# Kernel optimization log

Hardware: AMD Instinct MI355X
Metric: run time of the kernel (lower is better)

Reference implementation:

```python
import jax, jax.numpy as jnp
import numpy as np

EMBED_DIM = 512
N_HEADS = 8
HEAD_DIM = EMBED_DIM // N_HEADS


def setup_inputs() -> dict:
    key = jax.random.key(0)
    ks = jax.random.split(key, 8)
    B, S, D = 8, 2048, EMBED_DIM
    scale = 1.0 / np.sqrt(D)
    return {
        "key": jax.random.normal(ks[0], (B, S, D), dtype=jnp.float32),
        "query": jax.random.normal(ks[1], (B, S, D), dtype=jnp.float32),
        "value": jax.random.normal(ks[2], (B, S, D), dtype=jnp.float32),
        # nn.Linear stores weight as [out, in]; y = x @ W.T. We store W_T=[in,out].
        "Wq": jax.random.normal(ks[3], (D, D), dtype=jnp.float32) * scale,
        "Wk": jax.random.normal(ks[4], (D, D), dtype=jnp.float32) * scale,
        "Wv": jax.random.normal(ks[5], (D, D), dtype=jnp.float32) * scale,
        "Wo": jax.random.normal(ks[6], (D, D), dtype=jnp.float32) * scale,
        "bo": jax.random.normal(ks[7], (D,), dtype=jnp.float32) * scale,
    }


def reference(key, query, value, Wq, Wk, Wv, Wo, bo):
    B, S, D = key.shape
    Sq = query.shape[1]
    H, Hd = N_HEADS, HEAD_DIM
    # projections (no bias for q/k/v)
    q = (query @ Wq).reshape(B, Sq, H, Hd)
    k = (key @ Wk).reshape(B, S, H, Hd)
    v = (value @ Wv).reshape(B, S, H, Hd)
    # scores: [B, H, Sq, S]
    product = jnp.einsum("bqhd,bkhd->bhqk", q, k) / np.sqrt(Hd)
    scores = jax.nn.softmax(product, axis=-1)
    out = jnp.einsum("bhqk,bkhd->bqhd", scores, v).reshape(B, Sq, D)
    return out @ Wo + bo
```

## Files before the change

kernel.cpp:

```cpp
#include <hip/hip_runtime.h>

typedef _Float16 half8 __attribute__((ext_vector_type(8)));
typedef _Float16 half4 __attribute__((ext_vector_type(4)));
typedef __fp16 fp16x2 __attribute__((ext_vector_type(2)));
typedef float floatx16 __attribute__((ext_vector_type(16)));
typedef unsigned int uint2v __attribute__((ext_vector_type(2)));

#define MFMA_F16 __builtin_amdgcn_mfma_f32_32x32x16_f16

__device__ __forceinline__ float fast_exp2(float x) {
#if __has_builtin(__builtin_amdgcn_exp2f)
    return __builtin_amdgcn_exp2f(x);
#else
    return exp2f(x);
#endif
}

__device__ __forceinline__ half4 pack4(float a, float b, float c, float d) {
    union { fp16x2 p[2]; half4 h; } u;
    u.p[0] = __builtin_amdgcn_cvt_pkrtz(a, b);
    u.p[1] = __builtin_amdgcn_cvt_pkrtz(c, d);
    return u.h;
}

__device__ __forceinline__ unsigned int pk2(float a, float b) {
    union { fp16x2 p; unsigned int u; } v;
    v.p = __builtin_amdgcn_cvt_pkrtz(a, b);
    return v.u;
}

__device__ __forceinline__ half8 ld_frag_lds(const _Float16* p) {
    union { half8 v; half4 h[2]; } u;
    u.h[0] = *(const half4*)(p);
    u.h[1] = *(const half4*)(p + 4);
    return u.v;
}

__device__ __forceinline__ void tile_barrier() {
    asm volatile("s_waitcnt lgkmcnt(0)" ::: "memory");
    __builtin_amdgcn_s_barrier();
    asm volatile("" ::: "memory");
}

__device__ __forceinline__ half8 pv_frag(const unsigned int* w, int i0) {
    uint2v s0 = __builtin_amdgcn_permlane32_swap(w[2 * i0 + 0], w[2 * i0 + 2], false, false);
    uint2v s1 = __builtin_amdgcn_permlane32_swap(w[2 * i0 + 1], w[2 * i0 + 3], false, false);
    union { unsigned int u[4]; half8 h; } pu;
    pu.u[0] = s0[0];
    pu.u[1] = s1[0];
    pu.u[2] = s0[1];
    pu.u[3] = s1[1];
    return pu.h;
}

__global__ __launch_bounds__(256) void wcvt_kernel(const float* __restrict__ Wq,
                                                   const float* __restrict__ Wk,
                                                   const float* __restrict__ Wv,
                                                   const float* __restrict__ Wo,
                                                   _Float16* __restrict__ Wt) {
    __shared__ _Float16 T[64 * 68];
    const int bx   = blockIdx.x;
    const int wsel = bx >> 6;
    const int tile = bx & 63;
    const int to   = (tile >> 3) * 64;
    const int ti   = (tile & 7) * 64;
    const float* src = (wsel == 0) ? Wq : (wsel == 1) ? Wk : (wsel == 2) ? Wv : Wo;
    const int t = threadIdx.x;
    const int rloc = t >> 4, c4 = (t & 15) * 4;
#pragma unroll
    for (int m = 0; m < 4; m++) {
        int i = ti + rloc + 16 * m;
        float4 f = *(const float4*)(src + (size_t)i * 512 + to + c4);
        T[(c4 + 0) * 68 + rloc + 16 * m] = (_Float16)f.x;
        T[(c4 + 1) * 68 + rloc + 16 * m] = (_Float16)f.y;
        T[(c4 + 2) * 68 + rloc + 16 * m] = (_Float16)f.z;
        T[(c4 + 3) * 68 + rloc + 16 * m] = (_Float16)f.w;
    }
    __syncthreads();
    const int o_loc = t >> 2, ich = (t & 3) * 16;
    const _Float16* s = &T[o_loc * 68 + ich];
    _Float16* dst = Wt + (size_t)wsel * 262144 + (size_t)(to + o_loc) * 512 + ti + ich;
    half4 a0 = *(const half4*)(s);
    half4 a1 = *(const half4*)(s + 4);
    half4 a2 = *(const half4*)(s + 8);
    half4 a3 = *(const half4*)(s + 12);
    *(half4*)(dst)      = a0;
    *(half4*)(dst + 4)  = a1;
    *(half4*)(dst + 8)  = a2;
    *(half4*)(dst + 12) = a3;
}

__global__ __launch_bounds__(256, 3) void qkv_gemm(const float* __restrict__ query,
                                                   const float* __restrict__ key,
                                                   const float* __restrict__ value,
                                                   const _Float16* __restrict__ Wt,
                                                   _Float16* __restrict__ Qh,
                                                   _Float16* __restrict__ Kh,
                                                   _Float16* __restrict__ Vt,
                                                   float C1) {
    __shared__ _Float16 Alds[128 * 68];
    __shared__ _Float16 Blds[128 * 68];

    const int z = blockIdx.z;
    const float* A = (z == 0) ? query : (z == 1) ? key : value;
    const _Float16* W = Wt + (size_t)z * 262144;

    const int tid  = threadIdx.x;
    const int lane = tid & 63;
    const int w    = tid >> 6;
    const int l31  = lane & 31;
    const int lh   = lane >> 5;
    const int wm   = w >> 1;
    const int wn   = w & 1;
    const int n0   = blockIdx.x * 128;
    const int m0   = blockIdx.y * 128;
    const int crow = tid >> 3;
    const int ck8  = (tid & 7) * 8;

    floatx16 acc[2][2];
#pragma unroll
    for (int i = 0; i < 2; i++)
#pragma unroll
        for (int j = 0; j < 2; j++)
#pragma unroll
            for (int r = 0; r < 16; r++) acc[i][j][r] = 0.0f;

    float4 apre[4][2];
    int4   bpre[4];
#pragma unroll
    for (int i = 0; i < 4; i++) {
        const float* p = A + (size_t)(m0 + crow + 32 * i) * 512 + ck8;
        apre[i][0] = *(const float4*)(p);
        apre[i][1] = *(const float4*)(p + 4);
        bpre[i] = *(const int4*)(W + (size_t)(n0 + crow + 32 * i) * 512 + ck8);
    }

    for (int t = 0; t < 8; t++) {
        __syncthreads();
#pragma unroll
        for (int i = 0; i < 4; i++) {
            int r = crow + 32 * i;
            float4 f0 = apre[i][0], f1 = apre[i][1];
            *(half4*)&Alds[r * 68 + ck8]     = pack4(f0.x, f0.y, f0.z, f0.w);
            *(half4*)&Alds[r * 68 + ck8 + 4] = pack4(f1.x, f1.y, f1.z, f1.w);
            *(int2*)&Blds[r * 68 + ck8]      = make_int2(bpre[i].x, bpre[i].y);
            *(int2*)&Blds[r * 68 + ck8 + 4]  = make_int2(bpre[i].z, bpre[i].w);
        }
        __syncthreads();
        if (t < 7) {
            int ks2 = (t + 1) * 64;
#pragma unroll
            for (int i = 0; i < 4; i++) {
                const float* p = A + (size_t)(m0 + crow + 32 * i) * 512 + ks2 + ck8;
                apre[i][0] = *(const float4*)(p);
                apre[i][1] = *(const float4*)(p + 4);
                bpre[i] = *(const int4*)(W + (size_t)(n0 + crow + 32 * i) * 512 + ks2 + ck8);
            }
        }
#pragma unroll
        for (int kc = 0; kc < 4; kc++) {
            int kb = kc * 16 + lh * 8;
            half8 af[2], bf[2];
            af[0] = ld_frag_lds(&Alds[(wm * 64 + l31) * 68 + kb]);
            af[1] = ld_frag_lds(&Alds[(wm * 64 + 32 + l31) * 68 + kb]);
            bf[0] = ld_frag_lds(&Blds[(wn * 64 + l31) * 68 + kb]);
            bf[1] = ld_frag_lds(&Blds[(wn * 64 + 32 + l31) * 68 + kb]);
#pragma unroll
            for (int i = 0; i < 2; i++)
#pragma unroll
                for (int j = 0; j < 2; j++)
                    acc[i][j] = MFMA_F16(af[i], bf[j], acc[i][j], 0, 0, 0);
        }
    }

    const float oscale = (z == 0) ? C1 : 1.0f;
    _Float16* out01 = (z == 0) ? Qh : Kh;
#pragma unroll
    for (int i = 0; i < 2; i++) {
#pragma unroll
        for (int j = 0; j < 2; j++) {
            int gn    = n0 + wn * 64 + j * 32 + l31;
            int mbase = m0 + wm * 64 + i * 32 + 4 * lh;
            int h = gn >> 6, hd = gn & 63;
            if (z < 2) {
#pragma unroll
                for (int r = 0; r < 16; r++) {
                    int gm = mbase + (r & 3) + 8 * (r >> 2);
                    int b = gm >> 11, s = gm & 2047;
                    out01[(size_t)((b * 8 + h) * 2048 + s) * 64 + hd] =
                        (_Float16)(acc[i][j][r] * oscale);
                }
            } else {
#pragma unroll
                for (int g = 0; g < 4; g++) {
                    int gm = mbase + 8 * g;
                    int b = gm >> 11, s = gm & 2047;
                    *(half4*)&Vt[(size_t)((b * 8 + h) * 64 + hd) * 2048 + s] =
                        pack4(acc[i][j][4 * g + 0], acc[i][j][4 * g + 1],
                              acc[i][j][4 * g + 2], acc[i][j][4 * g + 3]);
                }
            }
        }
    }
}

__global__ __launch_bounds__(256, 3) void out_gemm(const _Float16* __restrict__ A,
                                                   const _Float16* __restrict__ W,
                                                   const float* __restrict__ bias,
                                                   float* __restrict__ out) {
    __shared__ _Float16 Alds[128 * 68];
    __shared__ _Float16 Blds[128 * 68];

    const int tid  = threadIdx.x;
    const int lane = tid & 63;
    const int w    = tid >> 6;
    const int l31  = lane & 31;
    const int lh   = lane >> 5;
    const int wm   = w >> 1;
    const int wn   = w & 1;
    const int n0   = blockIdx.x * 128;
    const int m0   = blockIdx.y * 128;
    const int crow = tid >> 3;
    const int ck8  = (tid & 7) * 8;

    floatx16 acc[2][2];
#pragma unroll
    for (int i = 0; i < 2; i++)
#pragma unroll
        for (int j = 0; j < 2; j++)
#pragma unroll
            for (int r = 0; r < 16; r++) acc[i][j][r] = 0.0f;

    int4 apre[4], bpre[4];
#pragma unroll
    for (int i = 0; i < 4; i++) {
        apre[i] = *(const int4*)(A + (size_t)(m0 + crow + 32 * i) * 512 + ck8);
        bpre[i] = *(const int4*)(W + (size_t)(n0 + crow + 32 * i) * 512 + ck8);
    }

    for (int t = 0; t < 8; t++) {
        __syncthreads();
#pragma unroll
        for (int i = 0; i < 4; i++) {
            int r = crow + 32 * i;
            *(int2*)&Alds[r * 68 + ck8]     = make_int2(apre[i].x, apre[i].y);
            *(int2*)&Alds[r * 68 + ck8 + 4] = make_int2(apre[i].z, apre[i].w);
            *(int2*)&Blds[r * 68 + ck8]     = make_int2(bpre[i].x, bpre[i].y);
            *(int2*)&Blds[r * 68 + ck8 + 4] = make_int2(bpre[i].z, bpre[i].w);
        }
        __syncthreads();
        if (t < 7) {
            int ks2 = (t + 1) * 64;
#pragma unroll
            for (int i = 0; i < 4; i++) {
                apre[i] = *(const int4*)(A + (size_t)(m0 + crow + 32 * i) * 512 + ks2 + ck8);
                bpre[i] = *(const int4*)(W + (size_t)(n0 + crow + 32 * i) * 512 + ks2 + ck8);
            }
        }
#pragma unroll
        for (int kc = 0; kc < 4; kc++) {
            int kb = kc * 16 + lh * 8;
            half8 af[2], bf[2];
            af[0] = ld_frag_lds(&Alds[(wm * 64 + l31) * 68 + kb]);
            af[1] = ld_frag_lds(&Alds[(wm * 64 + 32 + l31) * 68 + kb]);
            bf[0] = ld_frag_lds(&Blds[(wn * 64 + l31) * 68 + kb]);
            bf[1] = ld_frag_lds(&Blds[(wn * 64 + 32 + l31) * 68 + kb]);
#pragma unroll
            for (int i = 0; i < 2; i++)
#pragma unroll
                for (int j = 0; j < 2; j++)
                    acc[i][j] = MFMA_F16(af[i], bf[j], acc[i][j], 0, 0, 0);
        }
    }

#pragma unroll
    for (int i = 0; i < 2; i++) {
#pragma unroll
        for (int j = 0; j < 2; j++) {
            int gn    = n0 + wn * 64 + j * 32 + l31;
            int mbase = m0 + wm * 64 + i * 32 + 4 * lh;
            float bv = bias[gn];
#pragma unroll
            for (int r = 0; r < 16; r++) {
                int gm = mbase + (r & 3) + 8 * (r >> 2);
                out[(size_t)gm * 512 + gn] = acc[i][j][r] + bv;
            }
        }
    }
}

__global__ __launch_bounds__(256, 3) void attn_kernel(const _Float16* __restrict__ Qg,
                                                      const _Float16* __restrict__ Kg,
                                                      const _Float16* __restrict__ Vg,
                                                      _Float16* __restrict__ AO) {
    __shared__ _Float16 Kbuf[2][64 * 68];
    __shared__ _Float16 Vbuf[2][64 * 68];

    const int tid  = threadIdx.x;
    const int lane = tid & 63;
    const int w    = tid >> 6;
    const int l31  = lane & 31;
    const int lh   = lane >> 5;
    const int h    = blockIdx.y;
    const int b    = blockIdx.z;
    const int q0   = blockIdx.x * 128 + w * 32;

    const size_t bhoff = (size_t)(b * 8 + h) * (2048 * 64);
    const _Float16* Qbh = Qg + bhoff;
    const _Float16* Kbh = Kg + bhoff;
    const _Float16* Vbh = Vg + bhoff;

    const int c0row = tid >> 3, ck8 = (tid & 7) * 8;
    const int c1row = c0row + 32;

    half8 qf[4];
#pragma unroll
    for (int kc = 0; kc < 4; kc++)
        qf[kc] = *(const half8*)(Qbh + (size_t)(q0 + l31) * 64 + kc * 16 + lh * 8);

    floatx16 O[2];
#pragma unroll
    for (int i = 0; i < 2; i++)
#pragma unroll
        for (int r = 0; r < 16; r++) O[i][r] = 0.0f;
    float lsum = 0.0f;

    unsigned int w16[16];
    half8 vf[4][2];

    int4 kpre[2], vpre[2];
    kpre[0] = *(const int4*)(Kbh + c0row * 64 + ck8);
    kpre[1] = *(const int4*)(Kbh + c1row * 64 + ck8);
    vpre[0] = *(const int4*)(Vbh + (size_t)c0row * 2048 + ck8);
    vpre[1] = *(const int4*)(Vbh + (size_t)c1row * 2048 + ck8);
    *(int2*)&Kbuf[0][c0row * 68 + ck8]     = make_int2(kpre[0].x, kpre[0].y);
    *(int2*)&Kbuf[0][c0row * 68 + ck8 + 4] = make_int2(kpre[0].z, kpre[0].w);
    *(int2*)&Kbuf[0][c1row * 68 + ck8]     = make_int2(kpre[1].x, kpre[1].y);
    *(int2*)&Kbuf[0][c1row * 68 + ck8 + 4] = make_int2(kpre[1].z, kpre[1].w);
    *(int2*)&Vbuf[0][c0row * 68 + ck8]     = make_int2(vpre[0].x, vpre[0].y);
    *(int2*)&Vbuf[0][c0row * 68 + ck8 + 4] = make_int2(vpre[0].z, vpre[0].w);
    *(int2*)&Vbuf[0][c1row * 68 + ck8]     = make_int2(vpre[1].x, vpre[1].y);
    *(int2*)&Vbuf[0][c1row * 68 + ck8 + 4] = make_int2(vpre[1].z, vpre[1].w);
    kpre[0] = *(const int4*)(Kbh + 4096 + c0row * 64 + ck8);
    kpre[1] = *(const int4*)(Kbh + 4096 + c1row * 64 + ck8);
    vpre[0] = *(const int4*)(Vbh + 64 + (size_t)c0row * 2048 + ck8);
    vpre[1] = *(const int4*)(Vbh + 64 + (size_t)c1row * 2048 + ck8);
    tile_barrier();

    for (int kt = 0; kt < 32; kt++) {
        const int cur = kt & 1;
        const _Float16* Kc = Kbuf[cur];
        const _Float16* Vc = Vbuf[cur];

        if (kt > 0) {
            __builtin_amdgcn_s_setprio(1);
#pragma unroll
            for (int kc = 0; kc < 4; kc++) {
                int i0 = (kc >> 1) * 4 + (kc & 1) * 2;
                half8 pf = pv_frag(w16, i0);
                O[0] = MFMA_F16(vf[kc][0], pf, O[0], 0, 0, 0);
                O[1] = MFMA_F16(vf[kc][1], pf, O[1], 0, 0, 0);
            }
            __builtin_amdgcn_s_setprio(0);
        }

        if (kt < 31) {
            _Float16* Kd = Kbuf[cur ^ 1];
            _Float16* Vd = Vbuf[cur ^ 1];
            *(int2*)&Kd[c0row * 68 + ck8]     = make_int2(kpre[0].x, kpre[0].y);
            *(int2*)&Kd[c0row * 68 + ck8 + 4] = make_int2(kpre[0].z, kpre[0].w);
            *(int2*)&Kd[c1row * 68 + ck8]     = make_int2(kpre[1].x, kpre[1].y);
            *(int2*)&Kd[c1row * 68 + ck8 + 4] = make_int2(kpre[1].z, kpre[1].w);
            *(int2*)&Vd[c0row * 68 + ck8]     = make_int2(vpre[0].x, vpre[0].y);
            *(int2*)&Vd[c0row * 68 + ck8 + 4] = make_int2(vpre[0].z, vpre[0].w);
            *(int2*)&Vd[c1row * 68 + ck8]     = make_int2(vpre[1].x, vpre[1].y);
            *(int2*)&Vd[c1row * 68 + ck8 + 4] = make_int2(vpre[1].z, vpre[1].w);
        }
        if (kt < 30) {
            const _Float16* Ksrc = Kbh + (size_t)(kt + 2) * 4096;
            const _Float16* Vsrc = Vbh + (size_t)(kt + 2) * 64;
            kpre[0] = *(const int4*)(Ksrc + c0row * 64 + ck8);
            kpre[1] = *(const int4*)(Ksrc + c1row * 64 + ck8);
            vpre[0] = *(const int4*)(Vsrc + (size_t)c0row * 2048 + ck8);
            vpre[1] = *(const int4*)(Vsrc + (size_t)c1row * 2048 + ck8);
        }

#pragma unroll
        for (int kc = 0; kc < 4; kc++) {
            vf[kc][0] = ld_frag_lds(&Vc[(l31)*68      + kc * 16 + lh * 8]);
            vf[kc][1] = ld_frag_lds(&Vc[(32 + l31)*68 + kc * 16 + lh * 8]);
        }

        floatx16 Sf[2];
#pragma unroll
        for (int i = 0; i < 2; i++)
#pragma unroll
            for (int r = 0; r < 16; r++) Sf[i][r] = 0.0f;
        __builtin_amdgcn_s_setprio(1);
#pragma unroll
        for (int kc = 0; kc < 4; kc++) {
#pragma unroll
            for (int ms = 0; ms < 2; ms++) {
                half8 kf = ld_frag_lds(&Kc[(ms * 32 + l31) * 68 + kc * 16 + lh * 8]);
                Sf[ms] = MFMA_F16(kf, qf[kc], Sf[ms], 0, 0, 0);
            }
        }
        __builtin_amdgcn_s_setprio(0);

        float rsA = 0.0f, rsB = 0.0f;
#pragma unroll
        for (int i = 0; i < 8; i++) {
            int ms = i >> 2, g = i & 3;
            float p0 = fast_exp2(Sf[ms][4 * g + 0]);
            float p1 = fast_exp2(Sf[ms][4 * g + 1]);
            float p2 = fast_exp2(Sf[ms][4 * g + 2]);
            float p3 = fast_exp2(Sf[ms][4 * g + 3]);
            rsA += p0 + p1;
            rsB += p2 + p3;
            w16[2 * i + 0] = pk2(p0, p1);
            w16[2 * i + 1] = pk2(p2, p3);
        }
        lsum += rsA + rsB;

        tile_barrier();
    }

    __builtin_amdgcn_s_setprio(1);
#pragma unroll
    for (int kc = 0; kc < 4; kc++) {
        int i0 = (kc >> 1) * 4 + (kc & 1) * 2;
        half8 pf = pv_frag(w16, i0);
        O[0] = MFMA_F16(vf[kc][0], pf, O[0], 0, 0, 0);
        O[1] = MFMA_F16(vf[kc][1], pf, O[1], 0, 0, 0);
    }
    __builtin_amdgcn_s_setprio(0);

    lsum += __shfl_xor(lsum, 32);
    float inv = 1.0f / lsum;
    int q = q0 + l31;
#pragma unroll
    for (int hs = 0; hs < 2; hs++) {
#pragma unroll
        for (int g = 0; g < 4; g++) {
            *(half4*)&AO[(size_t)(b * 2048 + q) * 512 + h * 64 + hs * 32 + g * 8 + lh * 4] =
                pack4(O[hs][4 * g + 0] * inv, O[hs][4 * g + 1] * inv,
                      O[hs][4 * g + 2] * inv, O[hs][4 * g + 3] * inv);
        }
    }
}

extern "C" void kernel_launch(void* const* d_in, const int* in_sizes, int n_in,
                              void* d_out, int out_size, void* d_ws, size_t ws_size,
                              hipStream_t stream) {
    const float* key   = (const float*)d_in[0];
    const float* query = (const float*)d_in[1];
    const float* value = (const float*)d_in[2];
    const float* Wq    = (const float*)d_in[3];
    const float* Wk    = (const float*)d_in[4];
    const float* Wv    = (const float*)d_in[5];
    const float* Wo    = (const float*)d_in[6];
    const float* bo    = (const float*)d_in[7];

    _Float16* ws = (_Float16*)d_ws;
    _Float16* Wt = ws;
    _Float16* Qh = ws + 1048576;
    _Float16* Kh = Qh + 8388608;
    _Float16* Vt = Kh + 8388608;
    _Float16* AO = Vt + 8388608;

    const float C1 = 0.18033688011112042f;

    wcvt_kernel<<<dim3(256), dim3(256), 0, stream>>>(Wq, Wk, Wv, Wo, Wt);

    qkv_gemm<<<dim3(4, 128, 3), dim3(256), 0, stream>>>(query, key, value, Wt,
                                                        Qh, Kh, Vt, C1);

    attn_kernel<<<dim3(16, 8, 8), dim3(256), 0, stream>>>(Qh, Kh, Vt, AO);

    out_gemm<<<dim3(4, 128), dim3(256), 0, stream>>>(AO, Wt + 3 * 262144, bo,
                                                     (float*)d_out);
}
```

Measured before the change: 288.8 us.

## Load V fragments directly from global memory, dropping LDS staging for V

```diff
diff --git a/kernel.cpp b/kernel.cpp
--- a/kernel.cpp
+++ b/kernel.cpp
@@ -294,7 +294,6 @@
                                                       const _Float16* __restrict__ Vg,
                                                       _Float16* __restrict__ AO) {
     __shared__ _Float16 Kbuf[2][64 * 68];
-    __shared__ _Float16 Vbuf[2][64 * 68];
 
     const int tid  = threadIdx.x;
     const int lane = tid & 63;
@@ -310,6 +309,9 @@
     const _Float16* Kbh = Kg + bhoff;
     const _Float16* Vbh = Vg + bhoff;
 
+    const _Float16* Vrow0 = Vbh + (size_t)l31 * 2048 + lh * 8;
+    const _Float16* Vrow1 = Vbh + (size_t)(32 + l31) * 2048 + lh * 8;
+
     const int c0row = tid >> 3, ck8 = (tid & 7) * 8;
     const int c1row = c0row + 32;
 
@@ -328,67 +330,38 @@
     unsigned int w16[16];
     half8 vf[4][2];
 
-    int4 kpre[2], vpre[2];
+    int4 kpre[2];
     kpre[0] = *(const int4*)(Kbh + c0row * 64 + ck8);
     kpre[1] = *(const int4*)(Kbh + c1row * 64 + ck8);
-    vpre[0] = *(const int4*)(Vbh + (size_t)c0row * 2048 + ck8);
-    vpre[1] = *(const int4*)(Vbh + (size_t)c1row * 2048 + ck8);
     *(int2*)&Kbuf[0][c0row * 68 + ck8]     = make_int2(kpre[0].x, kpre[0].y);
     *(int2*)&Kbuf[0][c0row * 68 + ck8 + 4] = make_int2(kpre[0].z, kpre[0].w);
     *(int2*)&Kbuf[0][c1row * 68 + ck8]     = make_int2(kpre[1].x, kpre[1].y);
     *(int2*)&Kbuf[0][c1row * 68 + ck8 + 4] = make_int2(kpre[1].z, kpre[1].w);
-    *(int2*)&Vbuf[0][c0row * 68 + ck8]     = make_int2(vpre[0].x, vpre[0].y);
-    *(int2*)&Vbuf[0][c0row * 68 + ck8 + 4] = make_int2(vpre[0].z, vpre[0].w);
-    *(int2*)&Vbuf[0][c1row * 68 + ck8]     = make_int2(vpre[1].x, vpre[1].y);
-    *(int2*)&Vbuf[0][c1row * 68 + ck8 + 4] = make_int2(vpre[1].z, vpre[1].w);
     kpre[0] = *(const int4*)(Kbh + 4096 + c0row * 64 + ck8);
     kpre[1] = *(const int4*)(Kbh + 4096 + c1row * 64 + ck8);
-    vpre[0] = *(const int4*)(Vbh + 64 + (size_t)c0row * 2048 + ck8);
-    vpre[1] = *(const int4*)(Vbh + 64 + (size_t)c1row * 2048 + ck8);
     tile_barrier();
 
     for (int kt = 0; kt < 32; kt++) {
         const int cur = kt & 1;
         const _Float16* Kc = Kbuf[cur];
-        const _Float16* Vc = Vbuf[cur];
-
-        if (kt > 0) {
-            __builtin_amdgcn_s_setprio(1);
-#pragma unroll
-            for (int kc = 0; kc < 4; kc++) {
-                int i0 = (kc >> 1) * 4 + (kc & 1) * 2;
-                half8 pf = pv_frag(w16, i0);
-                O[0] = MFMA_F16(vf[kc][0], pf, O[0], 0, 0, 0);
-                O[1] = MFMA_F16(vf[kc][1], pf, O[1], 0, 0, 0);
-            }
-            __builtin_amdgcn_s_setprio(0);
+
+#pragma unroll
+        for (int kc = 0; kc < 4; kc++) {
+            vf[kc][0] = *(const half8*)(Vrow0 + kt * 64 + kc * 16);
+            vf[kc][1] = *(const half8*)(Vrow1 + kt * 64 + kc * 16);
         }
 
         if (kt < 31) {
             _Float16* Kd = Kbuf[cur ^ 1];
-            _Float16* Vd = Vbuf[cur ^ 1];
             *(int2*)&Kd[c0row * 68 + ck8]     = make_int2(kpre[0].x, kpre[0].y);
             *(int2*)&Kd[c0row * 68 + ck8 + 4] = make_int2(kpre[0].z, kpre[0].w);
             *(int2*)&Kd[c1row * 68 + ck8]     = make_int2(kpre[1].x, kpre[1].y);
             *(int2*)&Kd[c1row * 68 + ck8 + 4] = make_int2(kpre[1].z, kpre[1].w);
-            *(int2*)&Vd[c0row * 68 + ck8]     = make_int2(vpre[0].x, vpre[0].y);
-            *(int2*)&Vd[c0row * 68 + ck8 + 4] = make_int2(vpre[0].z, vpre[0].w);
-            *(int2*)&Vd[c1row * 68 + ck8]     = make_int2(vpre[1].x, vpre[1].y);
-            *(int2*)&Vd[c1row * 68 + ck8 + 4] = make_int2(vpre[1].z, vpre[1].w);
         }
         if (kt < 30) {
             const _Float16* Ksrc = Kbh + (size_t)(kt + 2) * 4096;
-            const _Float16* Vsrc = Vbh + (size_t)(kt + 2) * 64;
             kpre[0] = *(const int4*)(Ksrc + c0row * 64 + ck8);
             kpre[1] = *(const int4*)(Ksrc + c1row * 64 + ck8);
-            vpre[0] = *(const int4*)(Vsrc + (size_t)c0row * 2048 + ck8);
-            vpre[1] = *(const int4*)(Vsrc + (size_t)c1row * 2048 + ck8);
-        }
-
-#pragma unroll
-        for (int kc = 0; kc < 4; kc++) {
-            vf[kc][0] = ld_frag_lds(&Vc[(l31)*68      + kc * 16 + lh * 8]);
-            vf[kc][1] = ld_frag_lds(&Vc[(32 + l31)*68 + kc * 16 + lh * 8]);
         }
 
         floatx16 Sf[2];
@@ -396,7 +369,6 @@
         for (int i = 0; i < 2; i++)
 #pragma unroll
             for (int r = 0; r < 16; r++) Sf[i][r] = 0.0f;
-        __builtin_amdgcn_s_setprio(1);
 #pragma unroll
         for (int kc = 0; kc < 4; kc++) {
 #pragma unroll
@@ -405,7 +377,6 @@
                 Sf[ms] = MFMA_F16(kf, qf[kc], Sf[ms], 0, 0, 0);
             }
         }
-        __builtin_amdgcn_s_setprio(0);
 
         float rsA = 0.0f, rsB = 0.0f;
 #pragma unroll
@@ -422,18 +393,16 @@
         }
         lsum += rsA + rsB;
 
+#pragma unroll
+        for (int kc = 0; kc < 4; kc++) {
+            int i0 = (kc >> 1) * 4 + (kc & 1) * 2;
+            half8 pf = pv_frag(w16, i0);
+            O[0] = MFMA_F16(vf[kc][0], pf, O[0], 0, 0, 0);
+            O[1] = MFMA_F16(vf[kc][1], pf, O[1], 0, 0, 0);
+        }
+
         tile_barrier();
     }
-
-    __builtin_amdgcn_s_setprio(1);
-#pragma unroll
-    for (int kc = 0; kc < 4; kc++) {
-        int i0 = (kc >> 1) * 4 + (kc & 1) * 2;
-        half8 pf = pv_frag(w16, i0);
-        O[0] = MFMA_F16(vf[kc][0], pf, O[0], 0, 0, 0);
-        O[1] = MFMA_F16(vf[kc][1], pf, O[1], 0, 0, 0);
-    }
-    __builtin_amdgcn_s_setprio(0);
 
     lsum += __shfl_xor(lsum, 32);
     float inv = 1.0f / lsum;
```

Measured after the change: 343.4 us. +18.9%, slower.
